# Kernel optimization log

Measured on AMD Instinct MI355X. Metric: run time of the kernel, lower is better.

## Reference

```python
import jax, jax.numpy as jnp
import numpy as np

B, S, H, E, K = 4, 2048, 1024, 8, 2


def setup_inputs() -> dict:
    key = jax.random.key(0)
    k_hs, k_eo, k_w1, k_w2 = jax.random.split(key, 4)
    return {
        "hidden_states": jax.random.normal(k_hs, (B, S, H), dtype=jnp.float32),
        "expert_outputs": jax.random.normal(k_eo, (E, B, S, H), dtype=jnp.float32),
        "W1": jax.random.normal(k_w1, (H, H), dtype=jnp.float32) * 0.02,
        "b1": jnp.zeros((H,), dtype=jnp.float32),
        "W2": jax.random.normal(k_w2, (H, E), dtype=jnp.float32) * 0.02,
        "b2": jnp.zeros((E,), dtype=jnp.float32),
        "k": K,
    }


def reference(hidden_states, expert_outputs, W1, b1, W2, b2, k):
    # Router MLP (eval mode: dropout is identity, no noise)
    h = jax.nn.relu(hidden_states @ W1 + b1)          # [B,S,H]
    router_logits = h @ W2 + b2                        # [B,S,E]
    router_probs = jax.nn.softmax(router_logits, axis=-1)
    top_k_gates, top_k_indices = jax.lax.top_k(router_probs, k)  # [B,S,k]
    n_experts = expert_outputs.shape[0]
    # Scatter top-k gates into a dense [B,S,E] gate matrix (same math as the
    # per-expert masked accumulation in the torch loop)
    onehot = jax.nn.one_hot(top_k_indices, n_experts, dtype=top_k_gates.dtype)  # [B,S,k,E]
    gate_mat = jnp.einsum('bsk,bske->bse', top_k_gates, onehot)
    combined = jnp.einsum('bse,ebsd->bsd', gate_mat, expert_outputs)
    return combined
```

## Files before the change

kernel.cpp:

```cpp
#include <hip/hip_runtime.h>
#include <math.h>


#define H_DIM 1024
#define E_NUM 8

typedef __attribute__((ext_vector_type(8))) short s16x8;
typedef __attribute__((ext_vector_type(8))) unsigned short u16x8;
typedef __attribute__((ext_vector_type(4))) float f32x4;

__device__ __forceinline__ unsigned short f2bf(float x) {
    unsigned int u = __float_as_uint(x);
    unsigned int r = (u + 0x7FFFu + ((u >> 16) & 1u)) >> 16;
    return (unsigned short)r;
}
__device__ __forceinline__ float bf2f(unsigned short b) {
    return __uint_as_float(((unsigned int)b) << 16);
}
__device__ __forceinline__ void gload_lds16(const void* g, void* lds) {
    __builtin_amdgcn_global_load_lds(
        (const __attribute__((address_space(1))) void*)g,
        (__attribute__((address_space(3))) void*)lds, 16, 0, 0);
}

__global__ __launch_bounds__(256) void prep_fused_kernel(
    const float* __restrict__ A, const float* __restrict__ W,
    char* __restrict__ Aimg, char* __restrict__ Bimg)
{
    if (blockIdx.x < 4096) {
        int t = blockIdx.x * 256 + threadIdx.x;
        int m = t >> 7;
        int k = (t & 127) << 3;
        const float* src = A + ((size_t)m << 10) + k;
        float4 v0 = *reinterpret_cast<const float4*>(src);
        float4 v1 = *reinterpret_cast<const float4*>(src + 4);
        float xs[8] = {v0.x, v0.y, v0.z, v0.w, v1.x, v1.y, v1.z, v1.w};
        u16x8 hv, lv;
        #pragma unroll
        for (int j = 0; j < 8; ++j) {
            unsigned short h = f2bf(xs[j]);
            hv[j] = h;
            lv[j] = f2bf(xs[j] - bf2f(h));
        }
        int rb = m >> 7, mr = m & 127, kt = k >> 5, s = (k >> 3) & 3;
        char* base = Aimg + (((size_t)(rb * 32 + kt)) << 14) + mr * 128;
        *reinterpret_cast<u16x8*>(base + ((s ^ (mr & 7)) << 4)) = hv;
        *reinterpret_cast<u16x8*>(base + (((s + 4) ^ (mr & 7)) << 4)) = lv;
    } else {
        int t = (blockIdx.x - 4096) * 256 + threadIdx.x;
        int n = t & 1023;
        int k = (t >> 10) << 3;
        u16x8 hv, lv;
        #pragma unroll
        for (int j = 0; j < 8; ++j) {
            float x = W[((size_t)(k + j) << 10) + n];
            unsigned short h = f2bf(x);
            hv[j] = h;
            lv[j] = f2bf(x - bf2f(h));
        }
        int cb = n >> 7, nr = n & 127, kt = k >> 5, s = (k >> 3) & 3;
        char* base = Bimg + (((size_t)(cb * 32 + kt)) << 14) + nr * 128;
        *reinterpret_cast<u16x8*>(base + ((s ^ (nr & 7)) << 4)) = hv;
        *reinterpret_cast<u16x8*>(base + (((s + 4) ^ (nr & 7)) << 4)) = lv;
    }
}

#define MFMA_B16 __builtin_amdgcn_mfma_f32_16x16x32_bf16
#define W2T_OFS 32768
#define W2T_PITCH 272

__global__ __launch_bounds__(256, 3) void gemm1_logits_kernel(
    const char* __restrict__ Aimg, const char* __restrict__ Bimg,
    const float* __restrict__ bias, const float* __restrict__ W2,
    float* __restrict__ Plog)
{
    __shared__ char smem[39296];

    int bid = blockIdx.x;
    int swz = (bid & 7) * 64 + (bid >> 3);
    int rb = swz >> 3;
    int cb = swz & 7;

    int tid = threadIdx.x;
    int lane = tid & 63;
    int wave = tid >> 6;
    int wm = (wave >> 1) * 64;
    int wn = (wave & 1) * 64;
    int l15 = lane & 15, l4 = lane >> 4;

    const int col0g = cb * 128;
    for (int i = tid; i < 1632; i += 256)
        *reinterpret_cast<float*>(smem + W2T_OFS + i * 4) = 0.f;
    __syncthreads();
    {
        int e = tid & 7, c4 = tid >> 3;
        #pragma unroll
        for (int j = 0; j < 4; ++j) {
            int col = c4 * 4 + j;
            float w = W2[(size_t)(col0g + col) * E_NUM + e];
            unsigned short wh = f2bf(w);
            unsigned short wl = f2bf(w - bf2f(wh));
            *reinterpret_cast<unsigned short*>(smem + W2T_OFS + e * W2T_PITCH + col * 2) = wh;
            *reinterpret_cast<unsigned short*>(smem + W2T_OFS + (e + 8) * W2T_PITCH + col * 2) = wl;
        }
    }
    __syncthreads();

    int aoff_h[4], aoff_l[4], boff_h[4], boff_l[4];
    #pragma unroll
    for (int f = 0; f < 4; ++f) {
        int ar = wm + f * 16 + l15;
        aoff_h[f] = ar * 128 + ((l4 ^ (ar & 7)) << 4);
        aoff_l[f] = ar * 128 + (((l4 + 4) ^ (ar & 7)) << 4);
        int br = wn + f * 16 + l15;
        boff_h[f] = 16384 + br * 128 + ((l4 ^ (br & 7)) << 4);
        boff_l[f] = 16384 + br * 128 + (((l4 + 4) ^ (br & 7)) << 4);
    }

    const char* abase = Aimg + (size_t)rb * (32 * 16384);
    const char* bbase = Bimg + (size_t)cb * (32 * 16384);

    f32x4 acc[4][4];
    #pragma unroll
    for (int i = 0; i < 4; ++i)
        #pragma unroll
        for (int j = 0; j < 4; ++j)
            acc[i][j] = (f32x4){0.f, 0.f, 0.f, 0.f};

    for (int kt = 0; kt < 32; ++kt) {
        const char* ga = abase + (kt << 14);
        const char* gb = bbase + (kt << 14);
        int toff = tid << 4;
        #pragma unroll
        for (int r = 0; r < 4; ++r) {
            gload_lds16(ga + (r << 12) + toff, smem + (r << 12) + toff);
            gload_lds16(gb + (r << 12) + toff, smem + 16384 + (r << 12) + toff);
        }
        __syncthreads();

        s16x8 ah[4], al[4], bh[4], bl[4];
        #pragma unroll
        for (int f = 0; f < 4; ++f) {
            ah[f] = *reinterpret_cast<const s16x8*>(smem + aoff_h[f]);
            al[f] = *reinterpret_cast<const s16x8*>(smem + aoff_l[f]);
            bh[f] = *reinterpret_cast<const s16x8*>(smem + boff_h[f]);
            bl[f] = *reinterpret_cast<const s16x8*>(smem + boff_l[f]);
        }
        #pragma unroll
        for (int m = 0; m < 4; ++m)
            #pragma unroll
            for (int n = 0; n < 4; ++n)
                acc[m][n] = MFMA_B16(ah[m], bh[n], acc[m][n], 0, 0, 0);
        #pragma unroll
        for (int m = 0; m < 4; ++m)
            #pragma unroll
            for (int n = 0; n < 4; ++n)
                acc[m][n] = MFMA_B16(ah[m], bl[n], acc[m][n], 0, 0, 0);
        #pragma unroll
        for (int m = 0; m < 4; ++m)
            #pragma unroll
            for (int n = 0; n < 4; ++n)
                acc[m][n] = MFMA_B16(al[m], bh[n], acc[m][n], 0, 0, 0);
        __syncthreads();
    }

    float bcol[4];
    #pragma unroll
    for (int fn = 0; fn < 4; ++fn) bcol[fn] = bias[col0g + wn + fn * 16 + l15];

    f32x4 plog[2];
    plog[0] = (f32x4){0.f, 0.f, 0.f, 0.f};
    plog[1] = (f32x4){0.f, 0.f, 0.f, 0.f};

    #pragma unroll
    for (int ch = 0; ch < 2; ++ch) {
        if ((wave & 1) == ch) {
            #pragma unroll
            for (int fm = 0; fm < 4; ++fm)
                #pragma unroll
                for (int r = 0; r < 4; ++r) {
                    int row = wm + fm * 16 + l4 * 4 + r;
                    int rx = (row & 7) << 4;
                    #pragma unroll
                    for (int fn = 0; fn < 4; ++fn) {
                        float hv = fmaxf(acc[fm][fn][r] + bcol[fn], 0.f);
                        unsigned short hh = f2bf(hv);
                        unsigned short hl = f2bf(hv - bf2f(hh));
                        int byteoff = row * 128 + ((((fn * 16 + l15) * 2)) ^ rx);
                        *reinterpret_cast<unsigned short*>(smem + byteoff) = hh;
                        *reinterpret_cast<unsigned short*>(smem + 16384 + byteoff) = hl;
                    }
                }
        }
        __syncthreads();

        #pragma unroll
        for (int fmm = 0; fmm < 2; ++fmm) {
            int rowb = wave * 32 + fmm * 16 + l15;
            int rx = (rowb & 7) << 4;
            int rowbase = rowb * 128;
            #pragma unroll
            for (int kc = 0; kc < 2; ++kc) {
                int co = kc * 64 + l4 * 16;
                s16x8 ahi = *reinterpret_cast<const s16x8*>(smem + rowbase + (co ^ rx));
                s16x8 alo = *reinterpret_cast<const s16x8*>(smem + 16384 + rowbase + (co ^ rx));
                int wb = W2T_OFS + ch * 128 + kc * 64 + l4 * 16;
                s16x8 whi = *reinterpret_cast<const s16x8*>(smem + wb + l15 * W2T_PITCH);
                s16x8 wlo = *reinterpret_cast<const s16x8*>(smem + wb + (l15 + 8) * W2T_PITCH);
                plog[fmm] = MFMA_B16(ahi, whi, plog[fmm], 0, 0, 0);
                plog[fmm] = MFMA_B16(ahi, wlo, plog[fmm], 0, 0, 0);
                plog[fmm] = MFMA_B16(alo, whi, plog[fmm], 0, 0, 0);
            }
        }
        __syncthreads();
    }

    if (l15 < 8) {
        #pragma unroll
        for (int fmm = 0; fmm < 2; ++fmm) {
            int rowg = rb * 128 + wave * 32 + fmm * 16 + l4 * 4;
            #pragma unroll
            for (int r = 0; r < 4; ++r)
                Plog[((size_t)cb * 8192 + rowg + r) * E_NUM + l15] = plog[fmm][r];
        }
    }
}

__global__ __launch_bounds__(256) void route_combine2_kernel(
    const float* __restrict__ Plog, const float* __restrict__ b2,
    const float* __restrict__ EO, float* __restrict__ Out, int M)
{
    const int t = blockIdx.x;
    const int tid = threadIdx.x;

    __shared__ float s_logit[E_NUM];
    __shared__ float s_g[2];
    __shared__ int   s_e[2];

    if (tid < 64) {
        int cbi = tid >> 3, e = tid & 7;
        float v = Plog[((size_t)cbi * M + t) * E_NUM + e];
        v += __shfl_xor(v, 8, 64);
        v += __shfl_xor(v, 16, 64);
        v += __shfl_xor(v, 32, 64);
        if (tid < 8) s_logit[tid] = v + b2[tid];
    }
    __syncthreads();

    if (tid == 0) {
        float logits[E_NUM];
        #pragma unroll
        for (int e = 0; e < E_NUM; ++e) logits[e] = s_logit[e];
        float m = logits[0];
        #pragma unroll
        for (int e = 1; e < E_NUM; ++e) m = fmaxf(m, logits[e]);
        float p[E_NUM], ssum = 0.f;
        #pragma unroll
        for (int e = 0; e < E_NUM; ++e) { p[e] = expf(logits[e] - m); ssum += p[e]; }
        float inv = 1.f / ssum;
        #pragma unroll
        for (int e = 0; e < E_NUM; ++e) p[e] *= inv;
        int e0 = 0;
        #pragma unroll
        for (int e = 1; e < E_NUM; ++e) if (p[e] > p[e0]) e0 = e;
        int e1 = (e0 == 0) ? 1 : 0;
        #pragma unroll
        for (int e = 0; e < E_NUM; ++e)
            if (e != e0 && e != e1 && p[e] > p[e1]) e1 = e;
        s_g[0] = p[e0]; s_g[1] = p[e1];
        s_e[0] = e0;    s_e[1] = e1;
    }
    __syncthreads();

    const float g0 = s_g[0], g1 = s_g[1];
    const size_t base0 = ((size_t)s_e[0] * M + t) * H_DIM;
    const size_t base1 = ((size_t)s_e[1] * M + t) * H_DIM;
    const int d = tid * 4;
    float4 x0 = *reinterpret_cast<const float4*>(&EO[base0 + d]);
    float4 x1 = *reinterpret_cast<const float4*>(&EO[base1 + d]);
    float4 o;
    o.x = g0 * x0.x + g1 * x1.x;
    o.y = g0 * x0.y + g1 * x1.y;
    o.z = g0 * x0.z + g1 * x1.z;
    o.w = g0 * x0.w + g1 * x1.w;
    *reinterpret_cast<float4*>(&Out[(size_t)t * H_DIM + d]) = o;
}

#define BM 128
#define BN 128
#define BK 16
#define PAD_LD 132

__global__ __launch_bounds__(256) void gemm1_relu_kernel(
    const float* __restrict__ A, const float* __restrict__ W,
    const float* __restrict__ bias, float* __restrict__ Hout,
    int M, int N, int K)
{
    __shared__ float As[BK][PAD_LD];
    __shared__ float Bs[BK][PAD_LD];
    const int tid = threadIdx.x;
    const int tx = tid & 15;
    const int ty = tid >> 4;
    const int row0 = blockIdx.y * BM;
    const int col0 = blockIdx.x * BN;
    float acc[8][8];
    #pragma unroll
    for (int i = 0; i < 8; ++i)
        #pragma unroll
        for (int j = 0; j < 8; ++j) acc[i][j] = 0.f;
    const int a_row = tid >> 2;
    const int a_k4  = (tid & 3) * 4;
    const int b_col4 = (tid & 31) * 4;
    const int b_kk   = tid >> 5;
    for (int k0 = 0; k0 < K; k0 += BK) {
        #pragma unroll
        for (int half = 0; half < 2; ++half) {
            int r = a_row + half * 64;
            float4 av = *reinterpret_cast<const float4*>(&A[(size_t)(row0 + r) * K + k0 + a_k4]);
            As[a_k4 + 0][r] = av.x; As[a_k4 + 1][r] = av.y;
            As[a_k4 + 2][r] = av.z; As[a_k4 + 3][r] = av.w;
        }
        #pragma unroll
        for (int half = 0; half < 2; ++half) {
            int kk = b_kk + half * 8;
            float4 bv = *reinterpret_cast<const float4*>(&W[(size_t)(k0 + kk) * N + col0 + b_col4]);
            *reinterpret_cast<float4*>(&Bs[kk][b_col4]) = bv;
        }
        __syncthreads();
        #pragma unroll
        for (int k = 0; k < BK; ++k) {
            float4 a0 = *reinterpret_cast<const float4*>(&As[k][ty * 8]);
            float4 a1 = *reinterpret_cast<const float4*>(&As[k][ty * 8 + 4]);
            float4 b0 = *reinterpret_cast<const float4*>(&Bs[k][tx * 8]);
            float4 b1 = *reinterpret_cast<const float4*>(&Bs[k][tx * 8 + 4]);
            float a[8] = {a0.x, a0.y, a0.z, a0.w, a1.x, a1.y, a1.z, a1.w};
            float b[8] = {b0.x, b0.y, b0.z, b0.w, b1.x, b1.y, b1.z, b1.w};
            #pragma unroll
            for (int i = 0; i < 8; ++i)
                #pragma unroll
                for (int j = 0; j < 8; ++j)
                    acc[i][j] = fmaf(a[i], b[j], acc[i][j]);
        }
        __syncthreads();
    }
    #pragma unroll
    for (int i = 0; i < 8; ++i) {
        int row = row0 + ty * 8 + i;
        #pragma unroll
        for (int j4 = 0; j4 < 2; ++j4) {
            int col = col0 + tx * 8 + j4 * 4;
            float4 v;
            v.x = fmaxf(acc[i][j4 * 4 + 0] + bias[col + 0], 0.f);
            v.y = fmaxf(acc[i][j4 * 4 + 1] + bias[col + 1], 0.f);
            v.z = fmaxf(acc[i][j4 * 4 + 2] + bias[col + 2], 0.f);
            v.w = fmaxf(acc[i][j4 * 4 + 3] + bias[col + 3], 0.f);
            *reinterpret_cast<float4*>(&Hout[(size_t)row * N + col]) = v;
        }
    }
}

__global__ __launch_bounds__(256) void route_combine_kernel(
    const float* __restrict__ Hbuf, const float* __restrict__ W2,
    const float* __restrict__ b2, const float* __restrict__ EO,
    float* __restrict__ Out, int M)
{
    const int t = blockIdx.x;
    const int tid = threadIdx.x;
    const int lane = tid & 63;
    const int wave = tid >> 6;
    const float* hrow = Hbuf + (size_t)t * H_DIM;

    float part[E_NUM];
    #pragma unroll
    for (int e = 0; e < E_NUM; ++e) part[e] = 0.f;
    #pragma unroll
    for (int it = 0; it < H_DIM / 256; ++it) {
        int j = tid + it * 256;
        float hv = hrow[j];
        const float* w = W2 + (size_t)j * E_NUM;
        #pragma unroll
        for (int e = 0; e < E_NUM; ++e) part[e] = fmaf(hv, w[e], part[e]);
    }
    #pragma unroll
    for (int off = 32; off > 0; off >>= 1)
        #pragma unroll
        for (int e = 0; e < E_NUM; ++e)
            part[e] += __shfl_down(part[e], off, 64);

    __shared__ float sred[4][E_NUM];
    __shared__ float s_g[2];
    __shared__ int   s_e[2];
    if (lane == 0)
        #pragma unroll
        for (int e = 0; e < E_NUM; ++e) sred[wave][e] = part[e];
    __syncthreads();

    if (tid == 0) {
        float logits[E_NUM];
        #pragma unroll
        for (int e = 0; e < E_NUM; ++e)
            logits[e] = sred[0][e] + sred[1][e] + sred[2][e] + sred[3][e] + b2[e];
        float m = logits[0];
        #pragma unroll
        for (int e = 1; e < E_NUM; ++e) m = fmaxf(m, logits[e]);
        float p[E_NUM], ssum = 0.f;
        #pragma unroll
        for (int e = 0; e < E_NUM; ++e) { p[e] = expf(logits[e] - m); ssum += p[e]; }
        float inv = 1.f / ssum;
        #pragma unroll
        for (int e = 0; e < E_NUM; ++e) p[e] *= inv;
        int e0 = 0;
        #pragma unroll
        for (int e = 1; e < E_NUM; ++e) if (p[e] > p[e0]) e0 = e;
        int e1 = (e0 == 0) ? 1 : 0;
        #pragma unroll
        for (int e = 0; e < E_NUM; ++e)
            if (e != e0 && e != e1 && p[e] > p[e1]) e1 = e;
        s_g[0] = p[e0]; s_g[1] = p[e1];
        s_e[0] = e0;    s_e[1] = e1;
    }
    __syncthreads();

    const float g0 = s_g[0], g1 = s_g[1];
    const size_t base0 = ((size_t)s_e[0] * M + t) * H_DIM;
    const size_t base1 = ((size_t)s_e[1] * M + t) * H_DIM;
    const int d = tid * 4;
    float4 x0 = *reinterpret_cast<const float4*>(&EO[base0 + d]);
    float4 x1 = *reinterpret_cast<const float4*>(&EO[base1 + d]);
    float4 o;
    o.x = g0 * x0.x + g1 * x1.x;
    o.y = g0 * x0.y + g1 * x1.y;
    o.z = g0 * x0.z + g1 * x1.z;
    o.w = g0 * x0.w + g1 * x1.w;
    *reinterpret_cast<float4*>(&Out[(size_t)t * H_DIM + d]) = o;
}

extern "C" void kernel_launch(void* const* d_in, const int* in_sizes, int n_in,
                              void* d_out, int out_size, void* d_ws, size_t ws_size,
                              hipStream_t stream)
{
    const float* hs = (const float*)d_in[0];
    const float* EO = (const float*)d_in[1];
    const float* W1 = (const float*)d_in[2];
    const float* b1 = (const float*)d_in[3];
    const float* W2 = (const float*)d_in[4];
    const float* b2 = (const float*)d_in[5];

    const int M = in_sizes[0] / H_DIM;
    float* out = (float*)d_out;

    const size_t A_IMG = (size_t)64 * 32 * 16384;
    const size_t B_IMG = (size_t)8 * 32 * 16384;
    const size_t PART  = (size_t)8 * 8192 * 8 * 4;
    if (M == 8192 && ws_size >= A_IMG + B_IMG + PART) {
        char*  Aimg = (char*)d_ws;
        char*  Bimg = (char*)d_ws + A_IMG;
        float* Plog = (float*)((char*)d_ws + A_IMG + B_IMG);
        prep_fused_kernel<<<4096 + 512, 256, 0, stream>>>(hs, W1, Aimg, Bimg);
        gemm1_logits_kernel<<<512, 256, 0, stream>>>(Aimg, Bimg, b1, W2, Plog);
        route_combine2_kernel<<<M, 256, 0, stream>>>(Plog, b2, EO, out, M);
    } else {
        dim3 grid1(H_DIM / BN, M / BM);
        gemm1_relu_kernel<<<grid1, 256, 0, stream>>>(hs, W1, b1, out, M, H_DIM, H_DIM);
        route_combine_kernel<<<M, 256, 0, stream>>>(out, W2, b2, EO, out, M);
    }
}
```

Measured before the change: 82.53 us.

## Fuse routing and expert combine into GEMM kernel via last-block-per-row atomic counter

Removes the separate route_combine2 kernel launch. Each GEMM block atomically increments a per-row-block counter, and the last of the 8 column blocks to finish reduces the partial logits, runs softmax and top-2, and combines the expert outputs for its 128 rows. This saves a kernel launch and the tail between kernels, and lets the combine phase overlap with GEMM blocks still running. The cost is that the combine work now sits on only 64 blocks with one wave per token, which may limit memory parallelism. It also adds a memset launch to reset the counters.

```diff
diff --git a/kernel.cpp b/kernel.cpp
--- a/kernel.cpp
+++ b/kernel.cpp
@@ -68,13 +68,16 @@
 #define MFMA_B16 __builtin_amdgcn_mfma_f32_16x16x32_bf16
 #define W2T_OFS 32768
 #define W2T_PITCH 272
+#define FLAG_OFS 39296
 
 __global__ __launch_bounds__(256, 3) void gemm1_logits_kernel(
     const char* __restrict__ Aimg, const char* __restrict__ Bimg,
     const float* __restrict__ bias, const float* __restrict__ W2,
-    float* __restrict__ Plog)
+    float* __restrict__ Plog, const float* __restrict__ b2,
+    const float* __restrict__ EO, float* __restrict__ Out,
+    int* __restrict__ Cnt)
 {
-    __shared__ char smem[39296];
+    __shared__ char smem[39304];
 
     int bid = blockIdx.x;
     int swz = (bid & 7) * 64 + (bid >> 3);
@@ -224,66 +227,61 @@
                 Plog[((size_t)cb * 8192 + rowg + r) * E_NUM + l15] = plog[fmm][r];
         }
     }
-}
-
-__global__ __launch_bounds__(256) void route_combine2_kernel(
-    const float* __restrict__ Plog, const float* __restrict__ b2,
-    const float* __restrict__ EO, float* __restrict__ Out, int M)
-{
-    const int t = blockIdx.x;
-    const int tid = threadIdx.x;
-
-    __shared__ float s_logit[E_NUM];
-    __shared__ float s_g[2];
-    __shared__ int   s_e[2];
-
-    if (tid < 64) {
-        int cbi = tid >> 3, e = tid & 7;
-        float v = Plog[((size_t)cbi * M + t) * E_NUM + e];
-        v += __shfl_xor(v, 8, 64);
-        v += __shfl_xor(v, 16, 64);
-        v += __shfl_xor(v, 32, 64);
-        if (tid < 8) s_logit[tid] = v + b2[tid];
+
+    __threadfence();
+    if (tid == 0) {
+        int old = atomicAdd(&Cnt[rb], 1);
+        *reinterpret_cast<int*>(smem + FLAG_OFS) = (old == 7) ? 1 : 0;
     }
     __syncthreads();
-
-    if (tid == 0) {
-        float logits[E_NUM];
-        #pragma unroll
-        for (int e = 0; e < E_NUM; ++e) logits[e] = s_logit[e];
-        float m = logits[0];
-        #pragma unroll
-        for (int e = 1; e < E_NUM; ++e) m = fmaxf(m, logits[e]);
-        float p[E_NUM], ssum = 0.f;
-        #pragma unroll
-        for (int e = 0; e < E_NUM; ++e) { p[e] = expf(logits[e] - m); ssum += p[e]; }
-        float inv = 1.f / ssum;
-        #pragma unroll
-        for (int e = 0; e < E_NUM; ++e) p[e] *= inv;
-        int e0 = 0;
-        #pragma unroll
-        for (int e = 1; e < E_NUM; ++e) if (p[e] > p[e0]) e0 = e;
-        int e1 = (e0 == 0) ? 1 : 0;
-        #pragma unroll
-        for (int e = 0; e < E_NUM; ++e)
-            if (e != e0 && e != e1 && p[e] > p[e1]) e1 = e;
-        s_g[0] = p[e0]; s_g[1] = p[e1];
-        s_e[0] = e0;    s_e[1] = e1;
-    }
-    __syncthreads();
-
-    const float g0 = s_g[0], g1 = s_g[1];
-    const size_t base0 = ((size_t)s_e[0] * M + t) * H_DIM;
-    const size_t base1 = ((size_t)s_e[1] * M + t) * H_DIM;
-    const int d = tid * 4;
-    float4 x0 = *reinterpret_cast<const float4*>(&EO[base0 + d]);
-    float4 x1 = *reinterpret_cast<const float4*>(&EO[base1 + d]);
-    float4 o;
-    o.x = g0 * x0.x + g1 * x1.x;
-    o.y = g0 * x0.y + g1 * x1.y;
-    o.z = g0 * x0.z + g1 * x1.z;
-    o.w = g0 * x0.w + g1 * x1.w;
-    *reinterpret_cast<float4*>(&Out[(size_t)t * H_DIM + d]) = o;
+    if (*reinterpret_cast<const int*>(smem + FLAG_OFS)) {
+        __threadfence();
+        const int e = lane & 7;
+        const float b2e = b2[e];
+        for (int ti = wave; ti < 128; ti += 4) {
+            const int t = rb * 128 + ti;
+            float v = Plog[((size_t)(lane >> 3) * 8192 + t) * E_NUM + e];
+            v += __shfl_xor(v, 8, 64);
+            v += __shfl_xor(v, 16, 64);
+            v += __shfl_xor(v, 32, 64);
+            float logit = v + b2e;
+            float lg[8];
+            #pragma unroll
+            for (int q = 0; q < 8; ++q) lg[q] = __shfl(logit, q, 64);
+            float mx = lg[0];
+            #pragma unroll
+            for (int q = 1; q < 8; ++q) mx = fmaxf(mx, lg[q]);
+            float p[8], ssum = 0.f;
+            #pragma unroll
+            for (int q = 0; q < 8; ++q) { p[q] = expf(lg[q] - mx); ssum += p[q]; }
+            float inv = 1.f / ssum;
+            #pragma unroll
+            for (int q = 0; q < 8; ++q) p[q] *= inv;
+            int e0 = 0;
+            #pragma unroll
+            for (int q = 1; q < 8; ++q) if (p[q] > p[e0]) e0 = q;
+            int e1 = (e0 == 0) ? 1 : 0;
+            #pragma unroll
+            for (int q = 0; q < 8; ++q)
+                if (q != e0 && q != e1 && p[q] > p[e1]) e1 = q;
+            const float g0 = p[e0], g1 = p[e1];
+            const float* x0 = EO + ((size_t)e0 * 8192 + t) * H_DIM;
+            const float* x1 = EO + ((size_t)e1 * 8192 + t) * H_DIM;
+            float* orow = Out + (size_t)t * H_DIM;
+            #pragma unroll
+            for (int it4 = 0; it4 < 4; ++it4) {
+                int d = (it4 * 64 + lane) * 4;
+                float4 a = *reinterpret_cast<const float4*>(x0 + d);
+                float4 b = *reinterpret_cast<const float4*>(x1 + d);
+                float4 o;
+                o.x = g0 * a.x + g1 * b.x;
+                o.y = g0 * a.y + g1 * b.y;
+                o.z = g0 * a.z + g1 * b.z;
+                o.w = g0 * a.w + g1 * b.w;
+                *reinterpret_cast<float4*>(orow + d) = o;
+            }
+        }
+    }
 }
 
 #define BM 128
@@ -452,13 +450,16 @@
     const size_t A_IMG = (size_t)64 * 32 * 16384;
     const size_t B_IMG = (size_t)8 * 32 * 16384;
     const size_t PART  = (size_t)8 * 8192 * 8 * 4;
-    if (M == 8192 && ws_size >= A_IMG + B_IMG + PART) {
+    const size_t CNT   = 64 * sizeof(int);
+    if (M == 8192 && ws_size >= A_IMG + B_IMG + PART + CNT) {
         char*  Aimg = (char*)d_ws;
         char*  Bimg = (char*)d_ws + A_IMG;
         float* Plog = (float*)((char*)d_ws + A_IMG + B_IMG);
+        int*   Cnt  = (int*)((char*)d_ws + A_IMG + B_IMG + PART);
+        hipMemsetAsync(Cnt, 0, CNT, stream);
         prep_fused_kernel<<<4096 + 512, 256, 0, stream>>>(hs, W1, Aimg, Bimg);
-        gemm1_logits_kernel<<<512, 256, 0, stream>>>(Aimg, Bimg, b1, W2, Plog);
-        route_combine2_kernel<<<M, 256, 0, stream>>>(Plog, b2, EO, out, M);
+        gemm1_logits_kernel<<<512, 256, 0, stream>>>(Aimg, Bimg, b1, W2, Plog,
+                                                     b2, EO, out, Cnt);
     } else {
         dim3 grid1(H_DIM / BN, M / BM);
         gemm1_relu_kernel<<<grid1, 256, 0, stream>>>(hs, W1, b1, out, M, H_DIM, H_DIM);
```

New measurement: 181.2 us. 2.2x slower.

## Double-buffer LDS tiles in router GEMM to overlap global loads with MFMA

Applied to the files above, without the earlier changes.

Doubles the shared-memory tile area so the next K-tile of A and B is loaded asynchronously via global_load_lds while MFMAs run on the current buffer. A single wait-and-barrier per iteration replaces the two __syncthreads. This hides global load latency behind compute. In exchange LDS per block nearly doubles and launch bounds drop from 3 to 2 blocks per CU, reducing occupancy.

```diff
diff --git a/kernel.cpp b/kernel.cpp
--- a/kernel.cpp
+++ b/kernel.cpp
@@ -66,15 +66,15 @@
 }
 
 #define MFMA_B16 __builtin_amdgcn_mfma_f32_16x16x32_bf16
-#define W2T_OFS 32768
+#define W2T_OFS 65536
 #define W2T_PITCH 272
 
-__global__ __launch_bounds__(256, 3) void gemm1_logits_kernel(
+__global__ __launch_bounds__(256, 2) void gemm1_logits_kernel(
     const char* __restrict__ Aimg, const char* __restrict__ Bimg,
     const float* __restrict__ bias, const float* __restrict__ W2,
     float* __restrict__ Plog)
 {
-    __shared__ char smem[39296];
+    __shared__ char smem[72064];
 
     int bid = blockIdx.x;
     int swz = (bid & 7) * 64 + (bid >> 3);
@@ -113,12 +113,26 @@
         aoff_h[f] = ar * 128 + ((l4 ^ (ar & 7)) << 4);
         aoff_l[f] = ar * 128 + (((l4 + 4) ^ (ar & 7)) << 4);
         int br = wn + f * 16 + l15;
-        boff_h[f] = 16384 + br * 128 + ((l4 ^ (br & 7)) << 4);
-        boff_l[f] = 16384 + br * 128 + (((l4 + 4) ^ (br & 7)) << 4);
+        boff_h[f] = br * 128 + ((l4 ^ (br & 7)) << 4);
+        boff_l[f] = br * 128 + (((l4 + 4) ^ (br & 7)) << 4);
     }
 
     const char* abase = Aimg + (size_t)rb * (32 * 16384);
     const char* bbase = Bimg + (size_t)cb * (32 * 16384);
+    const int toff = tid << 4;
+
+#define STAGE(kt_, aO, bO) do {                                              \
+    const char* ga_ = abase + (((size_t)(kt_)) << 14);                       \
+    const char* gb_ = bbase + (((size_t)(kt_)) << 14);                       \
+    gload_lds16(ga_ + toff,         smem + (aO) + toff);                     \
+    gload_lds16(ga_ + 4096 + toff,  smem + (aO) + 4096 + toff);              \
+    gload_lds16(ga_ + 8192 + toff,  smem + (aO) + 8192 + toff);              \
+    gload_lds16(ga_ + 12288 + toff, smem + (aO) + 12288 + toff);             \
+    gload_lds16(gb_ + toff,         smem + (bO) + toff);                     \
+    gload_lds16(gb_ + 4096 + toff,  smem + (bO) + 4096 + toff);              \
+    gload_lds16(gb_ + 8192 + toff,  smem + (bO) + 8192 + toff);              \
+    gload_lds16(gb_ + 12288 + toff, smem + (bO) + 12288 + toff);             \
+} while (0)
 
     f32x4 acc[4][4];
     #pragma unroll
@@ -127,24 +141,25 @@
         for (int j = 0; j < 4; ++j)
             acc[i][j] = (f32x4){0.f, 0.f, 0.f, 0.f};
 
+    STAGE(0, 0, 32768);
+    asm volatile("s_waitcnt vmcnt(0)" ::: "memory");
+    asm volatile("s_barrier" ::: "memory");
+
     for (int kt = 0; kt < 32; ++kt) {
-        const char* ga = abase + (kt << 14);
-        const char* gb = bbase + (kt << 14);
-        int toff = tid << 4;
-        #pragma unroll
-        for (int r = 0; r < 4; ++r) {
-            gload_lds16(ga + (r << 12) + toff, smem + (r << 12) + toff);
-            gload_lds16(gb + (r << 12) + toff, smem + 16384 + (r << 12) + toff);
-        }
-        __syncthreads();
+        const int cur = kt & 1;
+        const char* As = smem + cur * 16384;
+        const char* Bs = smem + 32768 + cur * 16384;
+
+        if (kt < 31)
+            STAGE(kt + 1, (cur ^ 1) * 16384, 32768 + (cur ^ 1) * 16384);
 
         s16x8 ah[4], al[4], bh[4], bl[4];
         #pragma unroll
         for (int f = 0; f < 4; ++f) {
-            ah[f] = *reinterpret_cast<const s16x8*>(smem + aoff_h[f]);
-            al[f] = *reinterpret_cast<const s16x8*>(smem + aoff_l[f]);
-            bh[f] = *reinterpret_cast<const s16x8*>(smem + boff_h[f]);
-            bl[f] = *reinterpret_cast<const s16x8*>(smem + boff_l[f]);
+            ah[f] = *reinterpret_cast<const s16x8*>(As + aoff_h[f]);
+            al[f] = *reinterpret_cast<const s16x8*>(As + aoff_l[f]);
+            bh[f] = *reinterpret_cast<const s16x8*>(Bs + boff_h[f]);
+            bl[f] = *reinterpret_cast<const s16x8*>(Bs + boff_l[f]);
         }
         #pragma unroll
         for (int m = 0; m < 4; ++m)
@@ -161,8 +176,11 @@
             #pragma unroll
             for (int n = 0; n < 4; ++n)
                 acc[m][n] = MFMA_B16(al[m], bh[n], acc[m][n], 0, 0, 0);
-        __syncthreads();
-    }
+
+        asm volatile("s_waitcnt vmcnt(0)" ::: "memory");
+        asm volatile("s_barrier" ::: "memory");
+    }
+#undef STAGE
 
     float bcol[4];
     #pragma unroll
```

New measurement: 86.39 us. 1.05x slower.

## Enlarge GEMM1 tile to 256 rows with triple-buffered async LDS pipeline

Applied to the files above, without the earlier changes.

Reworks the router GEMM kernel to use 512 threads per block covering a 256x128 output tile, halving the grid to 256 blocks. It replaces the load-then-compute loop with a three-stage LDS ring. Global-to-LDS copies for the tile two steps ahead are issued between the three split-bf16 MFMA passes, gated by explicit vmcnt/lgkmcnt waits, raw barriers and wave priority boosts. The aim is to hide global load latency behind MFMA work and to reuse each B tile across more rows. In exchange the block now needs about 150KB of LDS, which limits each CU to one block, and there are more barriers per iteration.

```diff
diff --git a/kernel.cpp b/kernel.cpp
--- a/kernel.cpp
+++ b/kernel.cpp
@@ -66,37 +66,38 @@
 }
 
 #define MFMA_B16 __builtin_amdgcn_mfma_f32_16x16x32_bf16
-#define W2T_OFS 32768
+#define W2T_OFS 147456
 #define W2T_PITCH 272
 
-__global__ __launch_bounds__(256, 3) void gemm1_logits_kernel(
+__global__ __launch_bounds__(512, 2) void gemm1_logits_kernel(
     const char* __restrict__ Aimg, const char* __restrict__ Bimg,
     const float* __restrict__ bias, const float* __restrict__ W2,
     float* __restrict__ Plog)
 {
-    __shared__ char smem[39296];
-
-    int bid = blockIdx.x;
-    int swz = (bid & 7) * 64 + (bid >> 3);
-    int rb = swz >> 3;
-    int cb = swz & 7;
-
-    int tid = threadIdx.x;
-    int lane = tid & 63;
-    int wave = tid >> 6;
-    int wm = (wave >> 1) * 64;
-    int wn = (wave & 1) * 64;
-    int l15 = lane & 15, l4 = lane >> 4;
+    __shared__ char smem[153984];
+
+    const int bid = blockIdx.x;
+    const int swz = (bid & 7) * 32 + (bid >> 3);
+    const int rb2 = swz >> 3;
+    const int cb  = swz & 7;
+
+    const int tid = threadIdx.x;
+    const int lane = tid & 63;
+    const int wave = tid >> 6;
+    const int wm = (wave >> 1) * 64;
+    const int wn = (wave & 1) * 64;
+    const int l15 = lane & 15, l4 = lane >> 4;
+    const int toff = tid << 4;
 
     const int col0g = cb * 128;
-    for (int i = tid; i < 1632; i += 256)
+    for (int i = tid; i < 1632; i += 512)
         *reinterpret_cast<float*>(smem + W2T_OFS + i * 4) = 0.f;
     __syncthreads();
     {
-        int e = tid & 7, c4 = tid >> 3;
-        #pragma unroll
-        for (int j = 0; j < 4; ++j) {
-            int col = c4 * 4 + j;
+        int e = tid & 7, c2 = tid >> 3;
+        #pragma unroll
+        for (int j = 0; j < 2; ++j) {
+            int col = c2 * 2 + j;
             float w = W2[(size_t)(col0g + col) * E_NUM + e];
             unsigned short wh = f2bf(w);
             unsigned short wl = f2bf(w - bf2f(wh));
@@ -110,15 +111,29 @@
     #pragma unroll
     for (int f = 0; f < 4; ++f) {
         int ar = wm + f * 16 + l15;
-        aoff_h[f] = ar * 128 + ((l4 ^ (ar & 7)) << 4);
-        aoff_l[f] = ar * 128 + (((l4 + 4) ^ (ar & 7)) << 4);
+        int sub = (ar >> 7) << 14;
+        int arr = (ar & 127) * 128;
+        int arx = ar & 7;
+        aoff_h[f] = sub + arr + ((l4 ^ arx) << 4);
+        aoff_l[f] = sub + arr + (((l4 + 4) ^ arx) << 4);
         int br = wn + f * 16 + l15;
-        boff_h[f] = 16384 + br * 128 + ((l4 ^ (br & 7)) << 4);
-        boff_l[f] = 16384 + br * 128 + (((l4 + 4) ^ (br & 7)) << 4);
-    }
-
-    const char* abase = Aimg + (size_t)rb * (32 * 16384);
-    const char* bbase = Bimg + (size_t)cb * (32 * 16384);
+        int brx = br & 7;
+        boff_h[f] = br * 128 + ((l4 ^ brx) << 4);
+        boff_l[f] = br * 128 + (((l4 + 4) ^ brx) << 4);
+    }
+
+    const size_t atb = (size_t)(rb2 * 2) * 32;
+
+#define GA(s_, kt_) (Aimg + ((atb + (size_t)(s_) * 32 + (kt_)) << 14))
+#define GB(kt_)     (Bimg + (((size_t)cb * 32 + (kt_)) << 14))
+#define STAGE_A(kt_, s_, bO) do { const char* g_ = GA(s_, kt_);              \
+    gload_lds16(g_ + toff,        smem + (bO) + (s_) * 16384 + toff);        \
+    gload_lds16(g_ + 8192 + toff, smem + (bO) + (s_) * 16384 + 8192 + toff); \
+} while (0)
+#define STAGE_B(kt_, bO) do { const char* g_ = GB(kt_);                      \
+    gload_lds16(g_ + toff,        smem + (bO) + toff);                       \
+    gload_lds16(g_ + 8192 + toff, smem + (bO) + 8192 + toff);                \
+} while (0)
 
     f32x4 acc[4][4];
     #pragma unroll
@@ -127,42 +142,80 @@
         for (int j = 0; j < 4; ++j)
             acc[i][j] = (f32x4){0.f, 0.f, 0.f, 0.f};
 
-    for (int kt = 0; kt < 32; ++kt) {
-        const char* ga = abase + (kt << 14);
-        const char* gb = bbase + (kt << 14);
-        int toff = tid << 4;
-        #pragma unroll
-        for (int r = 0; r < 4; ++r) {
-            gload_lds16(ga + (r << 12) + toff, smem + (r << 12) + toff);
-            gload_lds16(gb + (r << 12) + toff, smem + 16384 + (r << 12) + toff);
-        }
-        __syncthreads();
-
-        s16x8 ah[4], al[4], bh[4], bl[4];
+    STAGE_A(0, 0, 0);      STAGE_A(0, 1, 0);      STAGE_B(0, 98304);
+    STAGE_A(1, 0, 32768);  STAGE_A(1, 1, 32768);  STAGE_B(1, 98304 + 16384);
+
+    int bi = 0;
+    for (int t = 0; t < 32; ++t) {
+        const char* As = smem + bi * 32768;
+        const char* Bs = smem + 98304 + bi * 16384;
+        int pi = bi + 2; if (pi >= 3) pi -= 3;
+        const int pA = pi * 32768;
+        const int pB = 98304 + pi * 16384;
+
+        if (t < 31) asm volatile("s_waitcnt vmcnt(6)" ::: "memory");
+        else        asm volatile("s_waitcnt vmcnt(0)" ::: "memory");
+        __builtin_amdgcn_s_barrier();
+
+        s16x8 ah[4], bh[4];
         #pragma unroll
         for (int f = 0; f < 4; ++f) {
-            ah[f] = *reinterpret_cast<const s16x8*>(smem + aoff_h[f]);
-            al[f] = *reinterpret_cast<const s16x8*>(smem + aoff_l[f]);
-            bh[f] = *reinterpret_cast<const s16x8*>(smem + boff_h[f]);
-            bl[f] = *reinterpret_cast<const s16x8*>(smem + boff_l[f]);
-        }
+            ah[f] = *reinterpret_cast<const s16x8*>(As + aoff_h[f]);
+            bh[f] = *reinterpret_cast<const s16x8*>(Bs + boff_h[f]);
+        }
+        if (t < 30) STAGE_A(t + 2, 0, pA);
+        __builtin_amdgcn_s_barrier();
+        asm volatile("s_waitcnt lgkmcnt(0)" ::: "memory");
+        __builtin_amdgcn_sched_barrier(0);
+        __builtin_amdgcn_s_setprio(1);
         #pragma unroll
         for (int m = 0; m < 4; ++m)
             #pragma unroll
             for (int n = 0; n < 4; ++n)
                 acc[m][n] = MFMA_B16(ah[m], bh[n], acc[m][n], 0, 0, 0);
+        __builtin_amdgcn_s_setprio(0);
+        __builtin_amdgcn_s_barrier();
+
+        s16x8 bl[4];
+        #pragma unroll
+        for (int f = 0; f < 4; ++f)
+            bl[f] = *reinterpret_cast<const s16x8*>(Bs + boff_l[f]);
+        if (t < 30) STAGE_A(t + 2, 1, pA);
+        __builtin_amdgcn_s_barrier();
+        asm volatile("s_waitcnt lgkmcnt(0)" ::: "memory");
+        __builtin_amdgcn_sched_barrier(0);
+        __builtin_amdgcn_s_setprio(1);
         #pragma unroll
         for (int m = 0; m < 4; ++m)
             #pragma unroll
             for (int n = 0; n < 4; ++n)
                 acc[m][n] = MFMA_B16(ah[m], bl[n], acc[m][n], 0, 0, 0);
+        __builtin_amdgcn_s_setprio(0);
+        __builtin_amdgcn_s_barrier();
+
+        s16x8 al[4];
+        #pragma unroll
+        for (int f = 0; f < 4; ++f)
+            al[f] = *reinterpret_cast<const s16x8*>(As + aoff_l[f]);
+        if (t < 30) STAGE_B(t + 2, pB);
+        __builtin_amdgcn_s_barrier();
+        asm volatile("s_waitcnt lgkmcnt(0)" ::: "memory");
+        __builtin_amdgcn_sched_barrier(0);
+        __builtin_amdgcn_s_setprio(1);
         #pragma unroll
         for (int m = 0; m < 4; ++m)
             #pragma unroll
             for (int n = 0; n < 4; ++n)
                 acc[m][n] = MFMA_B16(al[m], bh[n], acc[m][n], 0, 0, 0);
-        __syncthreads();
-    }
+        __builtin_amdgcn_s_setprio(0);
+        __builtin_amdgcn_s_barrier();
+
+        bi = bi + 1; if (bi >= 3) bi = 0;
+    }
+#undef STAGE_A
+#undef STAGE_B
+#undef GA
+#undef GB
 
     float bcol[4];
     #pragma unroll
@@ -188,7 +241,7 @@
                         unsigned short hl = f2bf(hv - bf2f(hh));
                         int byteoff = row * 128 + ((((fn * 16 + l15) * 2)) ^ rx);
                         *reinterpret_cast<unsigned short*>(smem + byteoff) = hh;
-                        *reinterpret_cast<unsigned short*>(smem + 16384 + byteoff) = hl;
+                        *reinterpret_cast<unsigned short*>(smem + 32768 + byteoff) = hl;
                     }
                 }
         }
@@ -203,7 +256,7 @@
             for (int kc = 0; kc < 2; ++kc) {
                 int co = kc * 64 + l4 * 16;
                 s16x8 ahi = *reinterpret_cast<const s16x8*>(smem + rowbase + (co ^ rx));
-                s16x8 alo = *reinterpret_cast<const s16x8*>(smem + 16384 + rowbase + (co ^ rx));
+                s16x8 alo = *reinterpret_cast<const s16x8*>(smem + 32768 + rowbase + (co ^ rx));
                 int wb = W2T_OFS + ch * 128 + kc * 64 + l4 * 16;
                 s16x8 whi = *reinterpret_cast<const s16x8*>(smem + wb + l15 * W2T_PITCH);
                 s16x8 wlo = *reinterpret_cast<const s16x8*>(smem + wb + (l15 + 8) * W2T_PITCH);
@@ -218,7 +271,7 @@
     if (l15 < 8) {
         #pragma unroll
         for (int fmm = 0; fmm < 2; ++fmm) {
-            int rowg = rb * 128 + wave * 32 + fmm * 16 + l4 * 4;
+            int rowg = rb2 * 256 + wave * 32 + fmm * 16 + l4 * 4;
             #pragma unroll
             for (int r = 0; r < 4; ++r)
                 Plog[((size_t)cb * 8192 + rowg + r) * E_NUM + l15] = plog[fmm][r];
@@ -457,7 +510,7 @@
         char*  Bimg = (char*)d_ws + A_IMG;
         float* Plog = (float*)((char*)d_ws + A_IMG + B_IMG);
         prep_fused_kernel<<<4096 + 512, 256, 0, stream>>>(hs, W1, Aimg, Bimg);
-        gemm1_logits_kernel<<<512, 256, 0, stream>>>(Aimg, Bimg, b1, W2, Plog);
+        gemm1_logits_kernel<<<256, 512, 0, stream>>>(Aimg, Bimg, b1, W2, Plog);
         route_combine2_kernel<<<M, 256, 0, stream>>>(Plog, b2, EO, out, M);
     } else {
         dim3 grid1(H_DIM / BN, M / BM);
```

Measured after the change: 85.94 us. +4.1%, slower.
